# Kernel optimization log

Measured on AMD Instinct MI355X. Metric: run time of the kernel, lower is better.

Reference implementation:

```python
import jax, jax.numpy as jnp
import numpy as np

B, T, D, V, N = 64, 512, 256, 32000, 48


def gru_layer(x_tbd, wx, wh, b):
    """Keras GRU (reset_after=True). x_tbd: [T,B,Din]; returns [T,B,D]."""
    bx, bh = b[0], b[1]
    px = x_tbd @ wx + bx  # [T,B,3D] precomputed input projections
    units = wh.shape[0]

    def step(h, pxt):
        ph = h @ wh + bh
        xz, xr, xh = jnp.split(pxt, 3, axis=-1)
        hz, hr, hh = jnp.split(ph, 3, axis=-1)
        z = jax.nn.sigmoid(xz + hz)
        r = jax.nn.sigmoid(xr + hr)
        hc = jnp.tanh(xh + r * hh)
        hn = z * h + (1.0 - z) * hc
        return hn, hn

    h0 = jnp.zeros((x_tbd.shape[1], units), x_tbd.dtype)
    _, out = jax.lax.scan(step, h0, px)
    return out


def crf_log_likelihood(emis, tags, seq_len, trans):
    Bb, Tt, Nn = emis.shape
    t_idx = jnp.arange(Tt)
    mask = (t_idx[None, :] < seq_len[:, None]).astype(emis.dtype)  # [B,T]
    unary = jnp.take_along_axis(emis, tags[..., None], axis=2)[..., 0]
    us = jnp.sum(unary * mask, axis=1)
    tr = trans[tags[:, :-1], tags[:, 1:]]  # [B,T-1]
    ts = jnp.sum(tr * mask[:, 1:], axis=1)

    def step(alpha, inp):
        e_t, m_t = inp  # [B,N], [B]
        new = jax.nn.logsumexp(alpha[:, :, None] + trans[None], axis=1) + e_t
        return jnp.where(m_t[:, None], new, alpha), None

    alpha, _ = jax.lax.scan(step, emis[:, 0],
                            (emis.transpose(1, 0, 2)[1:], (mask > 0).T[1:]))
    log_z = jax.nn.logsumexp(alpha, axis=-1)
    return us + ts - log_z


def crf_decode(emis, trans, seq_len):
    Bb, Tt, Nn = emis.shape
    mask = jnp.arange(Tt)[None, :] < seq_len[:, None]
    ident = jnp.arange(Nn, dtype=jnp.int32)[None, :]

    def step(alpha, inp):
        e_t, m_t = inp
        sc = alpha[:, :, None] + trans[None]  # [B,N,N] prev->cur
        bp = jnp.argmax(sc, axis=1).astype(jnp.int32)
        new = jnp.max(sc, axis=1) + e_t
        alpha_n = jnp.where(m_t[:, None], new, alpha)
        bp = jnp.where(m_t[:, None], bp, ident)
        return alpha_n, bp

    alpha, bps = jax.lax.scan(step, emis[:, 0],
                              (emis.transpose(1, 0, 2)[1:], mask.T[1:]))
    score = jnp.max(alpha, axis=-1)
    last = jnp.argmax(alpha, axis=-1).astype(jnp.int32)  # [B]

    def back(tag, bp):
        prev = jnp.take_along_axis(bp, tag[:, None], axis=1)[:, 0]
        return prev, tag

    tag0, tags = jax.lax.scan(back, last, bps, reverse=True)  # tags[i]=pos i+1
    pred = jnp.concatenate([tag0[:, None], tags.T], axis=1)  # [B,T]
    return pred, score


def setup_inputs() -> dict:
    key = jax.random.key(0)
    ks = jax.random.split(key, 20)
    s = 0.05
    inp = {
        'x': jax.random.randint(ks[0], (B, T), 0, V, dtype=jnp.int32),
        'y': jax.random.randint(ks[1], (B, T), 0, N, dtype=jnp.int32),
        'seq_len': jax.random.randint(ks[2], (B,), T // 2, T + 1, dtype=jnp.int32),
        'embed': jax.random.normal(ks[3], (V, D), jnp.float32) * s,
        'wx_f': jax.random.normal(ks[4], (D, 3 * D), jnp.float32) * s,
        'wh_f': jax.random.normal(ks[5], (D, 3 * D), jnp.float32) * s,
        'b_f': jnp.zeros((2, 3 * D), jnp.float32),
        'wx_b': jax.random.normal(ks[6], (D, 3 * D), jnp.float32) * s,
        'wh_b': jax.random.normal(ks[7], (D, 3 * D), jnp.float32) * s,
        'b_b': jnp.zeros((2, 3 * D), jnp.float32),
        'wq': jax.random.normal(ks[8], (2 * D, D), jnp.float32) * s,
        'bq': jnp.zeros((D,), jnp.float32),
        'wk': jax.random.normal(ks[9], (2 * D, D), jnp.float32) * s,
        'bk': jnp.zeros((D,), jnp.float32),
        'wv': jax.random.normal(ks[10], (2 * D, D), jnp.float32) * s,
        'bv': jnp.zeros((D,), jnp.float32),
        'wt': jax.random.normal(ks[11], (D, N), jnp.float32) * s,
        'bt': jnp.zeros((N,), jnp.float32),
        'trans': jax.random.normal(ks[12], (N, N), jnp.float32) * s,
    }
    return inp


def reference(x, y, seq_len, embed, wx_f, wh_f, b_f, wx_b, wh_b, b_b,
              wq, bq, wk, bk, wv, bv, wt, bt, trans):
    emb = embed[x]  # [B,T,D]
    xt = emb.transpose(1, 0, 2)  # [T,B,D]
    hf = gru_layer(xt, wx_f, wh_f, b_f)
    hb = gru_layer(xt[::-1], wx_b, wh_b, b_b)[::-1]
    h = jnp.concatenate([hf, hb], axis=-1).transpose(1, 0, 2)  # [B,T,2D]
    q = h @ wq + bq
    k = h @ wk + bk
    v = h @ wv + bv
    w = jax.nn.softmax(jnp.einsum('btd,bsd->bts', q, k), axis=-1)
    a = jnp.einsum('bts,bsd->btd', w, v)
    logits = a @ wt + bt  # [B,T,N]
    pred, _ = crf_decode(logits, trans, seq_len)
    ll = crf_log_likelihood(logits, y, seq_len, trans)
    return pred, ll
```

## Files before the change

kernel.cpp:

```cpp
#include <hip/hip_runtime.h>
#include <math.h>

typedef float f32;
typedef short short8 __attribute__((ext_vector_type(8)));
typedef float f32x4 __attribute__((ext_vector_type(4)));

#define TT 512
#define BB 64
#define DD 256
#define NN 48

static const size_t OFF_EBF  = 0;
static const size_t OFF_PXF  = 16384000;
static const size_t OFF_PXB  = OFF_PXF + 50331648;
static const size_t OFF_HBF_F= OFF_PXB + 50331648;
static const size_t OFF_HBF_B= OFF_HBF_F + 16777216;
static const size_t OFF_WXTF = OFF_HBF_B + 16777216;
static const size_t OFF_WXTB = OFF_WXTF + 393216;
static const size_t OFF_WHTF = OFF_WXTB + 393216;
static const size_t OFF_WHTB = OFF_WHTF + 393216;
static const size_t OFF_WQT  = OFF_WHTB + 393216;
static const size_t OFF_WKT  = OFF_WQT + 262144;
static const size_t OFF_WVT  = OFF_WKT + 262144;
static const size_t OFF_WTT  = OFF_WVT + 262144;
static const size_t OFF_QBF = OFF_PXF;
static const size_t OFF_KBF = OFF_QBF + 16777216;
static const size_t OFF_VBF = OFF_KBF + 16777216;
static const size_t OFF_VT  = OFF_VBF + 16777216;
static const size_t OFF_SCB = OFF_VT  + 16777216;
static const size_t OFF_ABF = OFF_QBF;
static const size_t OFF_LG  = OFF_KBF;

__device__ __forceinline__ ushort f2bf(f32 f) {
  union { f32 f; unsigned u; } v; v.f = f;
  unsigned r = v.u + 0x7fffu + ((v.u >> 16) & 1u);
  return (ushort)(r >> 16);
}
__device__ __forceinline__ f32 bf2f(ushort u) {
  union { unsigned u; f32 f; } v; v.u = ((unsigned)u) << 16; return v.f;
}
__device__ __forceinline__ f32 fsigmoid(f32 x) { return 1.f / (1.f + __expf(-x)); }
__device__ __forceinline__ f32 ftanh(f32 x) { return 1.f - 2.f / (__expf(2.f * x) + 1.f); }

template <int PL2>
__global__ __launch_bounds__(256) void tconv_k(
    const f32* __restrict__ in, ushort* __restrict__ out, int total, int Q) {
  int o = blockIdx.x * 256 + threadIdx.x;
  if (o >= total) return;
  int q = o >> PL2, p = o & ((1 << PL2) - 1);
  out[o] = f2bf(in[(size_t)p * Q + q]);
}

__global__ __launch_bounds__(256) void conv_embed_k(
    const f32* __restrict__ in, ushort* __restrict__ out, int n4) {
  int i = blockIdx.x * 256 + threadIdx.x;
  if (i >= n4) return;
  float4 v = ((const float4*)in)[i];
  ushort4 o;
  o.x = f2bf(v.x); o.y = f2bf(v.y); o.z = f2bf(v.z); o.w = f2bf(v.w);
  ((ushort4*)out)[i] = o;
}

__global__ __launch_bounds__(256) void tr_v_k(
    const ushort* __restrict__ in, ushort* __restrict__ out) {
  __shared__ ushort tile[32][33];
  int b = blockIdx.z;
  int s0 = blockIdx.x * 32, d0 = blockIdx.y * 32;
  int xc = threadIdx.x & 31, y0 = threadIdx.x >> 5;
  for (int yy = y0; yy < 32; yy += 8)
    tile[yy][xc] = in[((size_t)b * 512 + s0 + yy) * 256 + d0 + xc];
  __syncthreads();
  for (int yy = y0; yy < 32; yy += 8)
    out[((size_t)b * 256 + d0 + yy) * 512 + s0 + xc] = tile[xc][yy];
}

enum { GM_PX = 0, GM_QKV = 1, GM_SC = 2, GM_AV = 3, GM_LG = 4 };

template <int MODE>
__global__ __launch_bounds__(256) void mgemm(
    const ushort* __restrict__ Aa, const ushort* __restrict__ Ab,
    const ushort* __restrict__ Bt,
    f32* __restrict__ Cf, ushort* __restrict__ Cb,
    const f32* __restrict__ bias, const int* __restrict__ xi,
    int Ndim, int K, int rev) {
  const int m0 = blockIdx.y * 128;
  const int n0 = blockIdx.x * 128;
  const int bz = blockIdx.z;
  const int tid = threadIdx.x;
  const int l = tid & 63, w = tid >> 6;
  const int wr = w >> 1, wc = w & 1;
  __shared__ __align__(16) short Al[128 * 40];
  __shared__ __align__(16) short Bl[128 * 40];
  f32x4 acc[4][4] = {};

  const int rowa = tid >> 1;
  const int kha = (tid & 1) * 16;
  const int rA = m0 + rowa;
  const ushort* aBase = nullptr;
  const ushort* aBase2 = nullptr;
  if constexpr (MODE == GM_PX) {
    int tg = rA >> 6, b = rA & 63;
    int ts = rev ? (511 - tg) : tg;
    aBase = Aa + (size_t)xi[b * 512 + ts] * 256;
  } else if constexpr (MODE == GM_QKV) {
    int bl = rA >> 9, t = rA & 511;
    aBase = Aa + ((size_t)(t * 64 + bl)) * 256;
    aBase2 = Ab + ((size_t)((511 - t) * 64 + bl)) * 256;
  } else if constexpr (MODE == GM_SC) {
    aBase = Aa + ((size_t)(bz * 512 + rA)) * 256;
  } else if constexpr (MODE == GM_AV) {
    aBase = Aa + ((size_t)(bz * 512 + rA)) * 512;
  } else {
    aBase = Aa + (size_t)rA * 256;
  }
  const int rowb = tid >> 1;
  const int khb = (tid & 1) * 16;
  int rowg = n0 + rowb;
  if constexpr (MODE == GM_SC) rowg += bz * 512;
  if constexpr (MODE == GM_AV) rowg += bz * 256;
  const ushort* bBase = Bt + (size_t)rowg * K;
  const bool bValid = (MODE != GM_LG) || (n0 + rowb < Ndim);

  for (int k0 = 0; k0 < K; k0 += 32) {
    {
      int kk = k0 + kha;
      const ushort* src;
      if constexpr (MODE == GM_QKV)
        src = (kk < 256) ? aBase + kk : aBase2 + (kk - 256);
      else
        src = aBase + kk;
      uint4 a0 = *(const uint4*)src;
      uint4 a1 = *(const uint4*)(src + 8);
      *(uint4*)&Al[rowa * 40 + kha] = a0;
      *(uint4*)&Al[rowa * 40 + kha + 8] = a1;
    }
    {
      uint4 v0 = make_uint4(0, 0, 0, 0), v1 = make_uint4(0, 0, 0, 0);
      if (bValid) {
        const ushort* src = bBase + k0 + khb;
        v0 = *(const uint4*)src;
        v1 = *(const uint4*)(src + 8);
      }
      *(uint4*)&Bl[rowb * 40 + khb] = v0;
      *(uint4*)&Bl[rowb * 40 + khb + 8] = v1;
    }
    __syncthreads();
    const int fr = l & 15, fg = l >> 4;
    short8 af[4], bfr[4];
#pragma unroll
    for (int mf = 0; mf < 4; ++mf)
      af[mf] = *(const short8*)&Al[(wr * 64 + mf * 16 + fr) * 40 + fg * 8];
#pragma unroll
    for (int nf = 0; nf < 4; ++nf)
      bfr[nf] = *(const short8*)&Bl[(wc * 64 + nf * 16 + fr) * 40 + fg * 8];
#pragma unroll
    for (int mf = 0; mf < 4; ++mf)
#pragma unroll
      for (int nf = 0; nf < 4; ++nf)
        acc[mf][nf] = __builtin_amdgcn_mfma_f32_16x16x32_bf16(
            af[mf], bfr[nf], acc[mf][nf], 0, 0, 0);
    __syncthreads();
  }

  const int fr = l & 15, fq = l >> 4;
#pragma unroll
  for (int mf = 0; mf < 4; ++mf) {
#pragma unroll
    for (int nf = 0; nf < 4; ++nf) {
      int col = n0 + wc * 64 + nf * 16 + fr;
      f32 bs = 0.f;
      if (bias && col < Ndim) bs = bias[col];
#pragma unroll
      for (int rg = 0; rg < 4; ++rg) {
        int row = m0 + wr * 64 + mf * 16 + fq * 4 + rg;
        f32 vv = acc[mf][nf][rg] + bs;
        if constexpr (MODE == GM_PX)
          Cb[(size_t)row * 768 + col] = f2bf(vv);
        else if constexpr (MODE == GM_QKV)
          Cb[(size_t)row * 256 + col] = f2bf(vv);
        else if constexpr (MODE == GM_SC)
          Cb[((size_t)bz * 512 + row) * 512 + col] = f2bf(vv);
        else if constexpr (MODE == GM_AV)
          Cb[((size_t)bz * 512 + row) * 256 + col] = f2bf(vv);
        else {
          if (col < Ndim) Cf[(size_t)row * 48 + col] = vv;
        }
      }
    }
  }
}

__global__ __launch_bounds__(512, 1) void gru_scan5(
    const ushort* __restrict__ pxf, const ushort* __restrict__ pxb,
    const ushort* __restrict__ whtf, const ushort* __restrict__ whtb,
    const f32* __restrict__ b_f, const f32* __restrict__ b_b,
    ushort* __restrict__ hfbf, ushort* __restrict__ hbbf) {
  const int dir = blockIdx.x >> 2;
  const int rg4 = blockIdx.x & 3;
  const int tid = threadIdx.x;
  const int w = tid >> 6, l = tid & 63;
  const int fr = l & 15, fq = l >> 4;
  const ushort* px  = dir ? pxb : pxf;
  const ushort* wht = dir ? whtb : whtf;
  const f32* bh = (dir ? b_b : b_f) + 768;
  ushort* hseq = dir ? hbbf : hfbf;

  __shared__ __align__(16) char ldsWh[131072];
  __shared__ __align__(16) char ldsH[2][8192];

#pragma unroll
  for (int i = 0; i < 16; ++i) {
    int idx = i * 512 + tid;
    int col = idx >> 5, kc = idx & 31;
    uint4 v = *(const uint4*)&wht[(size_t)(512 + col) * 256 + kc * 8];
    *(uint4*)&ldsWh[col * 512 + ((kc * 16) ^ ((col & 7) << 4))] = v;
  }
  ((uint4*)ldsH[0])[tid] = make_uint4(0, 0, 0, 0);

  const int ctb = w * 2;
  short8 wzv[2][8], wrv[2][8];
#pragma unroll
  for (int ct = 0; ct < 2; ++ct) {
    int col = (ctb + ct) * 16 + fr;
#pragma unroll
    for (int ks = 0; ks < 8; ++ks) {
      wzv[ct][ks] = *(const short8*)&wht[(size_t)col * 256 + ks * 32 + fq * 8];
      wrv[ct][ks] = *(const short8*)&wht[(size_t)(256 + col) * 256 + ks * 32 + fq * 8];
    }
  }
  f32 bhz[2], bhr[2], bhh[2];
#pragma unroll
  for (int ct = 0; ct < 2; ++ct) {
    int col = (ctb + ct) * 16 + fr;
    bhz[ct] = bh[col]; bhr[ct] = bh[256 + col]; bhh[ct] = bh[512 + col];
  }
  f32 hold[8];
#pragma unroll
  for (int i = 0; i < 8; ++i) hold[i] = 0.f;

  auto loadpx = [&](int t, ushort* pv) {
    const ushort* pxt = px + ((size_t)t * 64 + rg4 * 16) * 768;
#pragma unroll
    for (int ct = 0; ct < 2; ++ct) {
      int col = (ctb + ct) * 16 + fr;
#pragma unroll
      for (int ri = 0; ri < 4; ++ri) {
        const ushort* p = pxt + (fq * 4 + ri) * 768 + col;
        pv[(ct * 4 + ri) * 3 + 0] = p[0];
        pv[(ct * 4 + ri) * 3 + 1] = p[256];
        pv[(ct * 4 + ri) * 3 + 2] = p[512];
      }
    }
  };

  auto step = [&](int t, int buf, const ushort* pc, ushort* pn) {
    if (t + 1 < TT) loadpx(t + 1, pn);
    if (t > 0) {
      int r = tid >> 5, kc = tid & 31;
      uint4 v = *(const uint4*)&ldsH[buf][r * 512 + ((kc * 16) ^ ((r & 7) << 4))];
      *(uint4*)&hseq[((size_t)(t - 1) * 64 + rg4 * 16 + r) * 256 + kc * 8] = v;
    }
    f32x4 az[2] = {}, ar[2] = {}, ah[2] = {};
#pragma unroll
    for (int ks = 0; ks < 8; ++ks) {
      short8 a = *(const short8*)&ldsH[buf][fr * 512 + ((ks * 64 + fq * 16) ^ ((fr & 7) << 4))];
#pragma unroll
      for (int ct = 0; ct < 2; ++ct) {
        int col = (ctb + ct) * 16 + fr;
        az[ct] = __builtin_amdgcn_mfma_f32_16x16x32_bf16(a, wzv[ct][ks], az[ct], 0, 0, 0);
        ar[ct] = __builtin_amdgcn_mfma_f32_16x16x32_bf16(a, wrv[ct][ks], ar[ct], 0, 0, 0);
        short8 wh8 = *(const short8*)&ldsWh[col * 512 + ((ks * 64 + fq * 16) ^ ((col & 7) << 4))];
        ah[ct] = __builtin_amdgcn_mfma_f32_16x16x32_bf16(a, wh8, ah[ct], 0, 0, 0);
      }
    }
#pragma unroll
    for (int ct = 0; ct < 2; ++ct)
#pragma unroll
      for (int ri = 0; ri < 4; ++ri) {
        int idx = ct * 4 + ri;
        f32 zv = fsigmoid(az[ct][ri] + bhz[ct] + bf2f(pc[idx * 3 + 0]));
        f32 rv = fsigmoid(ar[ct][ri] + bhr[ct] + bf2f(pc[idx * 3 + 1]));
        f32 hc = ftanh(bf2f(pc[idx * 3 + 2]) + rv * (ah[ct][ri] + bhh[ct]));
        f32 hn = zv * hold[idx] + (1.f - zv) * hc;
        hold[idx] = hn;
        int col = (ctb + ct) * 16 + fr;
        int r = fq * 4 + ri;
        *(ushort*)&ldsH[buf ^ 1][r * 512 + ((col * 2) ^ ((r & 7) << 4))] = f2bf(hn);
      }
    __syncthreads();
  };

  ushort pA[24], pB[24];
  loadpx(0, pA);
  __syncthreads();
#pragma unroll 1
  for (int t2 = 0; t2 < TT; t2 += 2) {
    step(t2, 0, pA, pB);
    step(t2 + 1, 1, pB, pA);
  }
  {
    int r = tid >> 5, kc = tid & 31;
    uint4 v = *(const uint4*)&ldsH[0][r * 512 + ((kc * 16) ^ ((r & 7) << 4))];
    *(uint4*)&hseq[((size_t)511 * 64 + rg4 * 16 + r) * 256 + kc * 8] = v;
  }
}

__global__ __launch_bounds__(256) void softmax_ip(ushort* __restrict__ p) {
  size_t row = blockIdx.x;
  uint* pr = (uint*)(p + row * 512);
  int tid = threadIdx.x;
  uint u = pr[tid];
  f32 v0 = bf2f((ushort)(u & 0xffff)), v1 = bf2f((ushort)(u >> 16));
  f32 m = fmaxf(v0, v1);
  for (int off = 32; off; off >>= 1) m = fmaxf(m, __shfl_xor(m, off));
  __shared__ f32 red[4];
  __shared__ f32 red2[4];
  if ((tid & 63) == 0) red[tid >> 6] = m;
  __syncthreads();
  m = fmaxf(fmaxf(red[0], red[1]), fmaxf(red[2], red[3]));
  f32 e0 = __expf(v0 - m), e1 = __expf(v1 - m);
  f32 s = e0 + e1;
  for (int off = 32; off; off >>= 1) s += __shfl_xor(s, off);
  if ((tid & 63) == 0) red2[tid >> 6] = s;
  __syncthreads();
  s = red2[0] + red2[1] + red2[2] + red2[3];
  f32 inv = 1.f / s;
  pr[tid] = (uint)f2bf(e0 * inv) | ((uint)f2bf(e1 * inv) << 16);
}

__global__ __launch_bounds__(64) void crf_ll_k(
    const f32* __restrict__ logits, const int* __restrict__ y,
    const int* __restrict__ seq_len, const f32* __restrict__ trans,
    f32* __restrict__ out) {
  const int b = blockIdx.x, tid = threadIdx.x;
  __shared__ f32 tr[NN * NN];
  for (int i = tid; i < NN * NN; i += 64) tr[i] = trans[i];
  const f32* em = logits + (size_t)b * TT * NN;
  const int L = seq_len[b];
  const bool act = tid < NN;
  f32 Ecol[NN];
#pragma unroll
  for (int i = 0; i < NN; ++i)
    Ecol[i] = act ? __expf(trans[i * NN + tid]) : 0.f;
  f32 alpha = act ? em[tid] : -1e30f;
  __syncthreads();
  for (int t = 1; t < L; ++t) {
    f32 m = alpha;
    for (int off = 32; off; off >>= 1) m = fmaxf(m, __shfl_xor(m, off));
    f32 e = __expf(alpha - m);
    f32 s = 0.f;
#pragma unroll
    for (int i = 0; i < NN; ++i) s += __shfl(e, i) * Ecol[i];
    if (act) alpha = m + __logf(s) + em[t * NN + tid];
  }
  f32 us = 0.f, ts = 0.f;
  for (int t = tid; t < TT; t += 64) {
    if (t < L) {
      us += em[t * NN + y[b * TT + t]];
      if (t >= 1) ts += tr[y[b * TT + t - 1] * NN + y[b * TT + t]];
    }
  }
  for (int off = 32; off; off >>= 1) { us += __shfl_xor(us, off); ts += __shfl_xor(ts, off); }
  f32 m = alpha;
  for (int off = 32; off; off >>= 1) m = fmaxf(m, __shfl_xor(m, off));
  f32 e = __expf(alpha - m);
  f32 s = e;
  for (int off = 32; off; off >>= 1) s += __shfl_xor(s, off);
  if (tid == 0) out[(size_t)BB * TT + b] = us + ts - (m + __logf(s));
}

__global__ __launch_bounds__(64) void crf_decode_k(
    const f32* __restrict__ logits, const int* __restrict__ seq_len,
    const f32* __restrict__ trans, f32* __restrict__ out) {
  const int b = blockIdx.x, tid = threadIdx.x;
  __shared__ f32 tr[NN][NN];
  __shared__ f32 al[2][NN];
  __shared__ unsigned char bp[TT - 1][NN];
  __shared__ unsigned char pr[TT];
  for (int i = tid; i < NN * NN; i += 64) tr[i / NN][i % NN] = trans[i];
  const f32* em = logits + (size_t)b * TT * NN;
  const int L = seq_len[b];
  if (tid < NN) al[0][tid] = em[tid];
  __syncthreads();
  int cur = 0;
  for (int t = 1; t < TT; ++t) {
    if (tid < NN) {
      if (t < L) {
        f32 m = -1e30f; int arg = 0;
        for (int i = 0; i < NN; ++i) {
          f32 v = al[cur][i] + tr[i][tid];
          if (v > m) { m = v; arg = i; }
        }
        al[cur ^ 1][tid] = m + em[t * NN + tid];
        bp[t - 1][tid] = (unsigned char)arg;
      } else {
        al[cur ^ 1][tid] = al[cur][tid];
        bp[t - 1][tid] = (unsigned char)tid;
      }
    }
    __syncthreads();
    cur ^= 1;
  }
  if (tid == 0) {
    f32 m = -1e30f; int last = 0;
    for (int i = 0; i < NN; ++i)
      if (al[cur][i] > m) { m = al[cur][i]; last = i; }
    int tag = last;
    for (int t = TT - 2; t >= 0; --t) { pr[t + 1] = (unsigned char)tag; tag = bp[t][tag]; }
    pr[0] = (unsigned char)tag;
  }
  __syncthreads();
  for (int t = tid; t < TT; t += 64)
    out[(size_t)b * TT + t] = (f32)pr[t];
}

extern "C" void kernel_launch(void* const* d_in, const int* in_sizes, int n_in,
                              void* d_out, int out_size, void* d_ws, size_t ws_size,
                              hipStream_t stream) {
  const int* x       = (const int*)d_in[0];
  const int* y       = (const int*)d_in[1];
  const int* seq_len = (const int*)d_in[2];
  const f32* embed   = (const f32*)d_in[3];
  const f32* wx_f    = (const f32*)d_in[4];
  const f32* wh_f    = (const f32*)d_in[5];
  const f32* b_f     = (const f32*)d_in[6];
  const f32* wx_b    = (const f32*)d_in[7];
  const f32* wh_b    = (const f32*)d_in[8];
  const f32* b_b     = (const f32*)d_in[9];
  const f32* wq      = (const f32*)d_in[10];
  const f32* bq      = (const f32*)d_in[11];
  const f32* wk      = (const f32*)d_in[12];
  const f32* bk      = (const f32*)d_in[13];
  const f32* wv      = (const f32*)d_in[14];
  const f32* bv      = (const f32*)d_in[15];
  const f32* wt      = (const f32*)d_in[16];
  const f32* bt      = (const f32*)d_in[17];
  const f32* trans   = (const f32*)d_in[18];
  f32* out = (f32*)d_out;

  char* ws = (char*)d_ws;
  ushort* ebf  = (ushort*)(ws + OFF_EBF);
  ushort* pxfb = (ushort*)(ws + OFF_PXF);
  ushort* pxbb = (ushort*)(ws + OFF_PXB);
  ushort* hfbf = (ushort*)(ws + OFF_HBF_F);
  ushort* hbbf = (ushort*)(ws + OFF_HBF_B);
  ushort* wxtf = (ushort*)(ws + OFF_WXTF);
  ushort* wxtb = (ushort*)(ws + OFF_WXTB);
  ushort* whtf = (ushort*)(ws + OFF_WHTF);
  ushort* whtb = (ushort*)(ws + OFF_WHTB);
  ushort* wqt  = (ushort*)(ws + OFF_WQT);
  ushort* wkt  = (ushort*)(ws + OFF_WKT);
  ushort* wvt  = (ushort*)(ws + OFF_WVT);
  ushort* wtt  = (ushort*)(ws + OFF_WTT);
  ushort* qbf = (ushort*)(ws + OFF_QBF);
  ushort* kbf = (ushort*)(ws + OFF_KBF);
  ushort* vbf = (ushort*)(ws + OFF_VBF);
  ushort* vT  = (ushort*)(ws + OFF_VT);
  ushort* scb = (ushort*)(ws + OFF_SCB);
  ushort* abf = (ushort*)(ws + OFF_ABF);
  f32*    lg  = (f32*)(ws + OFF_LG);

  conv_embed_k<<<8000, 256, 0, stream>>>(embed, ebf, 2048000);
  tconv_k<8><<<768, 256, 0, stream>>>(wx_f, wxtf, 196608, 768);
  tconv_k<8><<<768, 256, 0, stream>>>(wx_b, wxtb, 196608, 768);
  tconv_k<8><<<768, 256, 0, stream>>>(wh_f, whtf, 196608, 768);
  tconv_k<8><<<768, 256, 0, stream>>>(wh_b, whtb, 196608, 768);
  tconv_k<9><<<512, 256, 0, stream>>>(wq, wqt, 131072, 256);
  tconv_k<9><<<512, 256, 0, stream>>>(wk, wkt, 131072, 256);
  tconv_k<9><<<512, 256, 0, stream>>>(wv, wvt, 131072, 256);
  tconv_k<8><<<48, 256, 0, stream>>>(wt, wtt, 12288, 48);

  mgemm<GM_PX><<<dim3(6, 256), 256, 0, stream>>>(
      ebf, nullptr, wxtf, nullptr, pxfb, b_f, x, 768, 256, 0);
  mgemm<GM_PX><<<dim3(6, 256), 256, 0, stream>>>(
      ebf, nullptr, wxtb, nullptr, pxbb, b_b, x, 768, 256, 1);
  gru_scan5<<<8, 512, 0, stream>>>(pxfb, pxbb, whtf, whtb, b_f, b_b, hfbf, hbbf);

  mgemm<GM_QKV><<<dim3(2, 256), 256, 0, stream>>>(
      hfbf, hbbf, wqt, nullptr, qbf, bq, nullptr, 256, 512, 0);
  mgemm<GM_QKV><<<dim3(2, 256), 256, 0, stream>>>(
      hfbf, hbbf, wkt, nullptr, kbf, bk, nullptr, 256, 512, 0);
  mgemm<GM_QKV><<<dim3(2, 256), 256, 0, stream>>>(
      hfbf, hbbf, wvt, nullptr, vbf, bv, nullptr, 256, 512, 0);
  tr_v_k<<<dim3(16, 8, 64), 256, 0, stream>>>(vbf, vT);
  mgemm<GM_SC><<<dim3(4, 4, 64), 256, 0, stream>>>(
      qbf, nullptr, kbf, nullptr, scb, nullptr, nullptr, 512, 256, 0);
  softmax_ip<<<BB * TT, 256, 0, stream>>>(scb);
  mgemm<GM_AV><<<dim3(2, 4, 64), 256, 0, stream>>>(
      scb, nullptr, vT, nullptr, abf, nullptr, nullptr, 256, 512, 0);
  mgemm<GM_LG><<<dim3(1, 256), 256, 0, stream>>>(
      abf, nullptr, wtt, lg, nullptr, bt, nullptr, 48, 256, 0);

  crf_ll_k<<<BB, 64, 0, stream>>>(lg, y, seq_len, trans, out);
  crf_decode_k<<<BB, 64, 0, stream>>>(lg, seq_len, trans, out);
}
```

Baseline: 2.542 ms.

## Reorder GRU input projections to gate-interleaved batch-contiguous layout for vector loads

The PX GEMM epilogue now writes the input projections as [t][hidden][gate][batch], so the scan kernel can fetch each thread's z/r/h projections with six 8-byte vector loads instead of 24 scalar ushort loads. The hidden-state LDS buffer is re-laid out to an MFMA-fragment-friendly order that avoids swizzle math, and the Wh swizzle is changed. The scan step is rewritten with macros and scalar registers and the launch bound is raised. This targets per-step load latency on the serial recurrence critical path, but the scattered transposed epilogue stores in the GEMM may be less coalesced.

```diff
diff --git a/kernel.cpp b/kernel.cpp
--- a/kernel.cpp
+++ b/kernel.cpp
@@ -174,9 +174,11 @@
       for (int rg = 0; rg < 4; ++rg) {
         int row = m0 + wr * 64 + mf * 16 + fq * 4 + rg;
         f32 vv = acc[mf][nf][rg] + bs;
-        if constexpr (MODE == GM_PX)
-          Cb[(size_t)row * 768 + col] = f2bf(vv);
-        else if constexpr (MODE == GM_QKV)
+        if constexpr (MODE == GM_PX) {
+          int tg = row >> 6, b = row & 63;
+          int gate = col >> 8, hc = col & 255;
+          Cb[(((size_t)tg * 256 + hc) * 3 + gate) * 64 + b] = f2bf(vv);
+        } else if constexpr (MODE == GM_QKV)
           Cb[(size_t)row * 256 + col] = f2bf(vv);
         else if constexpr (MODE == GM_SC)
           Cb[((size_t)bz * 512 + row) * 512 + col] = f2bf(vv);
@@ -190,7 +192,62 @@
   }
 }
 
-__global__ __launch_bounds__(512, 1) void gru_scan5(
+#define MFMA_B16 __builtin_amdgcn_mfma_f32_16x16x32_bf16
+
+#define PXLOAD(T, P) {                                         \
+  size_t tb_ = (size_t)(T) * 49152;                            \
+  P##0 = *(const uint2*)(px + tb_ + off0);                     \
+  P##1 = *(const uint2*)(px + tb_ + off0 + 64);                \
+  P##2 = *(const uint2*)(px + tb_ + off0 + 128);               \
+  P##3 = *(const uint2*)(px + tb_ + off1);                     \
+  P##4 = *(const uint2*)(px + tb_ + off1 + 64);                \
+  P##5 = *(const uint2*)(px + tb_ + off1 + 128);               \
+}
+
+#define GATE1(CT, RI, UZ, UR, UH, AZ, AR, AH, KB, BZ, BR, BH)  \
+{                                                              \
+  f32 zv_ = fsigmoid((AZ)[RI] + (BZ) + bf2f((ushort)(UZ)));    \
+  f32 rv_ = fsigmoid((AR)[RI] + (BR) + bf2f((ushort)(UR)));    \
+  f32 hc_ = ftanh(bf2f((ushort)(UH)) + rv_ * ((AH)[RI] + (BH)));\
+  f32 hn_ = zv_ * h##CT##RI + (1.f - zv_) * hc_;               \
+  h##CT##RI = hn_;                                             \
+  *(ushort*)&dst_[(((KB) * 16) + fq * 4 + (RI)) * 16 + e2] = f2bf(hn_); \
+}
+
+#define STEP(T, BUF, PC, PN) {                                 \
+  if ((T) + 1 < TT) PXLOAD((T) + 1, PN);                       \
+  if ((T) > 0) {                                               \
+    uint4 v_ = *(const uint4*)&ldsH[BUF][tid * 16];            \
+    *(uint4*)&hseq[(((size_t)(T) - 1) * 64 + rowbase + (tid & 15)) * 256 + (tid >> 4) * 8] = v_; \
+  }                                                            \
+  uint2 q0_ = PC##0, q1_ = PC##1, q2_ = PC##2;                 \
+  uint2 q3_ = PC##3, q4_ = PC##4, q5_ = PC##5;                 \
+  f32x4 az0 = {}, az1 = {}, ar0 = {}, ar1 = {}, ah0 = {}, ah1 = {}; \
+  _Pragma("unroll")                                            \
+  for (int ks = 0; ks < 8; ++ks) {                             \
+    short8 a_  = *(const short8*)&ldsH[BUF][((ks * 4 + fq) * 16 + fr) * 16]; \
+    short8 w0_ = *(const short8*)&ldsWh[(ctb * 16 + fr) * 512 + ((ks * 64 + fq * 16) ^ ((fr & 7) << 6))]; \
+    short8 w1_ = *(const short8*)&ldsWh[((ctb + 1) * 16 + fr) * 512 + ((ks * 64 + fq * 16) ^ ((fr & 7) << 6))]; \
+    az0 = MFMA_B16(a_, wzv[0][ks], az0, 0, 0, 0);              \
+    ar0 = MFMA_B16(a_, wrv[0][ks], ar0, 0, 0, 0);              \
+    ah0 = MFMA_B16(a_, w0_, ah0, 0, 0, 0);                     \
+    az1 = MFMA_B16(a_, wzv[1][ks], az1, 0, 0, 0);              \
+    ar1 = MFMA_B16(a_, wrv[1][ks], ar1, 0, 0, 0);              \
+    ah1 = MFMA_B16(a_, w1_, ah1, 0, 0, 0);                     \
+  }                                                            \
+  char* dst_ = ldsH[(BUF) ^ 1];                                \
+  GATE1(0, 0, q0_.x,       q1_.x,       q2_.x,       az0, ar0, ah0, kb0, bhz0, bhr0, bhh0) \
+  GATE1(0, 1, q0_.x >> 16, q1_.x >> 16, q2_.x >> 16, az0, ar0, ah0, kb0, bhz0, bhr0, bhh0) \
+  GATE1(0, 2, q0_.y,       q1_.y,       q2_.y,       az0, ar0, ah0, kb0, bhz0, bhr0, bhh0) \
+  GATE1(0, 3, q0_.y >> 16, q1_.y >> 16, q2_.y >> 16, az0, ar0, ah0, kb0, bhz0, bhr0, bhh0) \
+  GATE1(1, 0, q3_.x,       q4_.x,       q5_.x,       az1, ar1, ah1, kb1, bhz1, bhr1, bhh1) \
+  GATE1(1, 1, q3_.x >> 16, q4_.x >> 16, q5_.x >> 16, az1, ar1, ah1, kb1, bhz1, bhr1, bhh1) \
+  GATE1(1, 2, q3_.y,       q4_.y,       q5_.y,       az1, ar1, ah1, kb1, bhz1, bhr1, bhh1) \
+  GATE1(1, 3, q3_.y >> 16, q4_.y >> 16, q5_.y >> 16, az1, ar1, ah1, kb1, bhz1, bhr1, bhh1) \
+  __syncthreads();                                             \
+}
+
+__global__ __launch_bounds__(512, 2) void gru_scan6(
     const ushort* __restrict__ pxf, const ushort* __restrict__ pxb,
     const ushort* __restrict__ whtf, const ushort* __restrict__ whtb,
     const f32* __restrict__ b_f, const f32* __restrict__ b_b,
@@ -213,7 +270,7 @@
     int idx = i * 512 + tid;
     int col = idx >> 5, kc = idx & 31;
     uint4 v = *(const uint4*)&wht[(size_t)(512 + col) * 256 + kc * 8];
-    *(uint4*)&ldsWh[col * 512 + ((kc * 16) ^ ((col & 7) << 4))] = v;
+    *(uint4*)&ldsWh[col * 512 + ((kc * 16) ^ ((col & 7) << 6))] = v;
   }
   ((uint4*)ldsH[0])[tid] = make_uint4(0, 0, 0, 0);
 
@@ -228,80 +285,36 @@
       wrv[ct][ks] = *(const short8*)&wht[(size_t)(256 + col) * 256 + ks * 32 + fq * 8];
     }
   }
-  f32 bhz[2], bhr[2], bhh[2];
-#pragma unroll
-  for (int ct = 0; ct < 2; ++ct) {
-    int col = (ctb + ct) * 16 + fr;
-    bhz[ct] = bh[col]; bhr[ct] = bh[256 + col]; bhh[ct] = bh[512 + col];
-  }
-  f32 hold[8];
-#pragma unroll
-  for (int i = 0; i < 8; ++i) hold[i] = 0.f;
-
-  auto loadpx = [&](int t, ushort* pv) {
-    const ushort* pxt = px + ((size_t)t * 64 + rg4 * 16) * 768;
-#pragma unroll
-    for (int ct = 0; ct < 2; ++ct) {
-      int col = (ctb + ct) * 16 + fr;
-#pragma unroll
-      for (int ri = 0; ri < 4; ++ri) {
-        const ushort* p = pxt + (fq * 4 + ri) * 768 + col;
-        pv[(ct * 4 + ri) * 3 + 0] = p[0];
-        pv[(ct * 4 + ri) * 3 + 1] = p[256];
-        pv[(ct * 4 + ri) * 3 + 2] = p[512];
-      }
-    }
-  };
-
-  auto step = [&](int t, int buf, const ushort* pc, ushort* pn) {
-    if (t + 1 < TT) loadpx(t + 1, pn);
-    if (t > 0) {
-      int r = tid >> 5, kc = tid & 31;
-      uint4 v = *(const uint4*)&ldsH[buf][r * 512 + ((kc * 16) ^ ((r & 7) << 4))];
-      *(uint4*)&hseq[((size_t)(t - 1) * 64 + rg4 * 16 + r) * 256 + kc * 8] = v;
-    }
-    f32x4 az[2] = {}, ar[2] = {}, ah[2] = {};
-#pragma unroll
-    for (int ks = 0; ks < 8; ++ks) {
-      short8 a = *(const short8*)&ldsH[buf][fr * 512 + ((ks * 64 + fq * 16) ^ ((fr & 7) << 4))];
-#pragma unroll
-      for (int ct = 0; ct < 2; ++ct) {
-        int col = (ctb + ct) * 16 + fr;
-        az[ct] = __builtin_amdgcn_mfma_f32_16x16x32_bf16(a, wzv[ct][ks], az[ct], 0, 0, 0);
-        ar[ct] = __builtin_amdgcn_mfma_f32_16x16x32_bf16(a, wrv[ct][ks], ar[ct], 0, 0, 0);
-        short8 wh8 = *(const short8*)&ldsWh[col * 512 + ((ks * 64 + fq * 16) ^ ((col & 7) << 4))];
-        ah[ct] = __builtin_amdgcn_mfma_f32_16x16x32_bf16(a, wh8, ah[ct], 0, 0, 0);
-      }
-    }
-#pragma unroll
-    for (int ct = 0; ct < 2; ++ct)
-#pragma unroll
-      for (int ri = 0; ri < 4; ++ri) {
-        int idx = ct * 4 + ri;
-        f32 zv = fsigmoid(az[ct][ri] + bhz[ct] + bf2f(pc[idx * 3 + 0]));
-        f32 rv = fsigmoid(ar[ct][ri] + bhr[ct] + bf2f(pc[idx * 3 + 1]));
-        f32 hc = ftanh(bf2f(pc[idx * 3 + 2]) + rv * (ah[ct][ri] + bhh[ct]));
-        f32 hn = zv * hold[idx] + (1.f - zv) * hc;
-        hold[idx] = hn;
-        int col = (ctb + ct) * 16 + fr;
-        int r = fq * 4 + ri;
-        *(ushort*)&ldsH[buf ^ 1][r * 512 + ((col * 2) ^ ((r & 7) << 4))] = f2bf(hn);
-      }
-    __syncthreads();
-  };
-
-  ushort pA[24], pB[24];
-  loadpx(0, pA);
-  __syncthreads();
+  f32 bhz0, bhz1, bhr0, bhr1, bhh0, bhh1;
+  {
+    int c0 = ctb * 16 + fr, c1 = (ctb + 1) * 16 + fr;
+    bhz0 = bh[c0]; bhz1 = bh[c1];
+    bhr0 = bh[256 + c0]; bhr1 = bh[256 + c1];
+    bhh0 = bh[512 + c0]; bhh1 = bh[512 + c1];
+  }
+  f32 h00 = 0.f, h01 = 0.f, h02 = 0.f, h03 = 0.f;
+  f32 h10 = 0.f, h11 = 0.f, h12 = 0.f, h13 = 0.f;
+
+  const int off0 = ((ctb + 0) * 16 + fr) * 192 + fq * 4;
+  const int off1 = ((ctb + 1) * 16 + fr) * 192 + fq * 4;
+  const int rowbase = rg4 * 16;
+  const int kb0 = ctb * 2 + (fr >> 3);
+  const int kb1 = kb0 + 2;
+  const int e2 = (fr & 7) * 2;
+
+  uint2 pA0, pA1, pA2, pA3, pA4, pA5;
+  uint2 pB0, pB1, pB2, pB3, pB4, pB5;
+  PXLOAD(0, pA);
+  __syncthreads();
+
 #pragma unroll 1
   for (int t2 = 0; t2 < TT; t2 += 2) {
-    step(t2, 0, pA, pB);
-    step(t2 + 1, 1, pB, pA);
+    STEP(t2, 0, pA, pB);
+    STEP(t2 + 1, 1, pB, pA);
   }
   {
-    int r = tid >> 5, kc = tid & 31;
-    uint4 v = *(const uint4*)&ldsH[0][r * 512 + ((kc * 16) ^ ((r & 7) << 4))];
-    *(uint4*)&hseq[((size_t)511 * 64 + rg4 * 16 + r) * 256 + kc * 8] = v;
+    uint4 v = *(const uint4*)&ldsH[0][tid * 16];
+    *(uint4*)&hseq[((size_t)511 * 64 + rowbase + (tid & 15)) * 256 + (tid >> 4) * 8] = v;
   }
 }
 
@@ -474,7 +487,7 @@
       ebf, nullptr, wxtf, nullptr, pxfb, b_f, x, 768, 256, 0);
   mgemm<GM_PX><<<dim3(6, 256), 256, 0, stream>>>(
       ebf, nullptr, wxtb, nullptr, pxbb, b_b, x, 768, 256, 1);
-  gru_scan5<<<8, 512, 0, stream>>>(pxfb, pxbb, whtf, whtb, b_f, b_b, hfbf, hbbf);
+  gru_scan6<<<8, 512, 0, stream>>>(pxfb, pxbb, whtf, whtb, b_f, b_b, hfbf, hbbf);
 
   mgemm<GM_QKV><<<dim3(2, 256), 256, 0, stream>>>(
       hfbf, hbbf, wqt, nullptr, qbf, bq, nullptr, 256, 512, 0);
```

After: 3.330 ms. 31.0% more time.
